# Optimization experiments

Hardware: AMD Instinct MI355X
Metric: run time of the kernel (lower is better)

Reference implementation:

```python
import jax, jax.numpy as jnp
import numpy as np

B, S, DIM = 2, 2048, 2048
H, DH = 16, 128
FF = 4 * DIM
EPS = 1e-5


def layer_norm(x, w, b, eps=EPS):
    m = jnp.mean(x, axis=-1, keepdims=True)
    v = jnp.mean(jnp.square(x - m), axis=-1, keepdims=True)
    return (x - m) * jax.lax.rsqrt(v + eps) * w + b


def apply_rotary(x, cos, sin):
    # x: [B, H, S, DH]; cos/sin: [S, DH//2]; complex multiply on (even, odd) pairs
    x2 = x.reshape(*x.shape[:-1], DH // 2, 2)
    x0, x1 = x2[..., 0], x2[..., 1]
    c = cos[None, None, :, :]
    s = sin[None, None, :, :]
    r0 = x0 * c - x1 * s
    r1 = x0 * s + x1 * c
    return jnp.stack([r0, r1], axis=-1).reshape(x.shape)


def setup_inputs() -> dict:
    key = jax.random.key(0)
    ks = jax.random.split(key, 16)
    sc = 0.02
    pos = jnp.arange(S, dtype=jnp.float32)[:, None]
    inv_freq = 1.0 / (10000.0 ** (jnp.arange(0, DH // 2, dtype=jnp.float32) / (DH // 2)))
    ang = pos * inv_freq[None, :]
    return {
        "hidden_states": jax.random.normal(ks[0], (B, S, DIM), jnp.float32),
        "freqs_cos": jnp.cos(ang),
        "freqs_sin": jnp.sin(ang),
        "wq": jax.random.normal(ks[1], (DIM, H * DH), jnp.float32) * sc,
        "wk": jax.random.normal(ks[2], (DIM, H * DH), jnp.float32) * sc,
        "wv": jax.random.normal(ks[3], (DIM, H * DH), jnp.float32) * sc,
        "nq_w": jnp.ones((DH,), jnp.float32),
        "nq_b": jnp.zeros((DH,), jnp.float32),
        "nk_w": jnp.ones((DH,), jnp.float32),
        "nk_b": jnp.zeros((DH,), jnp.float32),
        "wo": jax.random.normal(ks[4], (H * DH, DIM), jnp.float32) * sc,
        "bo": jnp.zeros((DIM,), jnp.float32),
        "ln1_w": jnp.ones((DIM,), jnp.float32),
        "ln1_b": jnp.zeros((DIM,), jnp.float32),
        "ln3_w": jnp.ones((DIM,), jnp.float32),
        "ln3_b": jnp.zeros((DIM,), jnp.float32),
        "w1": jax.random.normal(ks[5], (DIM, FF), jnp.float32) * sc,
        "b1": jnp.zeros((FF,), jnp.float32),
        "w2": jax.random.normal(ks[6], (FF, DIM), jnp.float32) * sc,
        "b2": jnp.zeros((DIM,), jnp.float32),
    }


def reference(hidden_states, freqs_cos, freqs_sin, wq, wk, wv, nq_w, nq_b, nk_w, nk_b,
              wo, bo, ln1_w, ln1_b, ln3_w, ln3_b, w1, b1, w2, b2):
    x = hidden_states
    # --- self-attention branch ---
    n = layer_norm(x, ln1_w, ln1_b)                       # [B,S,DIM]
    q = (n @ wq).reshape(B, S, H, DH)
    k = (n @ wk).reshape(B, S, H, DH)
    v = (n @ wv).reshape(B, S, H, DH)
    # per-head QK LayerNorm (norm over dim_head)
    q = layer_norm(q, nq_w, nq_b)
    k = layer_norm(k, nk_w, nk_b)
    q = q.transpose(0, 2, 1, 3)                            # [B,H,S,DH]
    k = k.transpose(0, 2, 1, 3)
    v = v.transpose(0, 2, 1, 3)
    q = apply_rotary(q, freqs_cos, freqs_sin)
    k = apply_rotary(k, freqs_cos, freqs_sin)
    scale = DH ** -0.5
    scores = jnp.einsum("bhqd,bhkd->bhqk", q, k) * scale   # [B,H,S,S]
    probs = jax.nn.softmax(scores, axis=-1)
    attn = jnp.einsum("bhqk,bhkd->bhqd", probs, v)         # [B,H,S,DH]
    attn = attn.transpose(0, 2, 1, 3).reshape(B, S, H * DH)
    x = x + (attn @ wo + bo)
    # --- feed-forward branch ---
    n = layer_norm(x, ln3_w, ln3_b)
    h = jax.nn.gelu(n @ w1 + b1, approximate=False)
    x = x + (h @ w2 + b2)
    return x
```

## Files before the change

### kernel.cpp

```cpp
#include <hip/hip_runtime.h>
#include <hip/hip_bf16.h>
#include <stdint.h>

typedef __hip_bfloat16 bf16;
typedef float v4f __attribute__((ext_vector_type(4)));
typedef short v8s __attribute__((ext_vector_type(8)));

#define DEV __device__ __forceinline__

DEV float b2f(bf16 x) { return __bfloat162float(x); }
DEV bf16 f2b(float x) { return __float2bfloat16(x); }

DEV void load4(const float* p, float* f) {
  float4 t = *(const float4*)p;
  f[0] = t.x; f[1] = t.y; f[2] = t.z; f[3] = t.w;
}
DEV void load4(const bf16* p, float* f) {
  union { uint2 u; bf16 h[4]; } t;
  t.u = *(const uint2*)p;
#pragma unroll
  for (int i = 0; i < 4; i++) f[i] = b2f(t.h[i]);
}
DEV void load8(const float* p, float* f) {
  float4 a = ((const float4*)p)[0], b = ((const float4*)p)[1];
  f[0] = a.x; f[1] = a.y; f[2] = a.z; f[3] = a.w;
  f[4] = b.x; f[5] = b.y; f[6] = b.z; f[7] = b.w;
}
DEV void load8(const bf16* p, float* f) {
  union { uint4 u; bf16 h[8]; } t;
  t.u = *(const uint4*)p;
#pragma unroll
  for (int i = 0; i < 8; i++) f[i] = b2f(t.h[i]);
}
DEV void store4(bf16* p, const float* f) {
  union { uint2 u; bf16 h[4]; } t;
#pragma unroll
  for (int i = 0; i < 4; i++) t.h[i] = f2b(f[i]);
  *(uint2*)p = t.u;
}
DEV void store4(float* p, const float* f) {
  *(float4*)p = make_float4(f[0], f[1], f[2], f[3]);
}

DEV void gld_lds16(const bf16* g, bf16* l) {
  auto gp = reinterpret_cast<const __attribute__((address_space(1))) uint32_t*>(
      reinterpret_cast<uintptr_t>(g));
  auto lp = reinterpret_cast<__attribute__((address_space(3))) uint32_t*>(
      reinterpret_cast<uintptr_t>(l));
  __builtin_amdgcn_global_load_lds(gp, lp, 16, 0, 0);
}

template <typename XT>
__global__ __launch_bounds__(256)
void ln2048_kernel(const XT* __restrict__ x, const float* __restrict__ w,
                   const float* __restrict__ b, bf16* __restrict__ y) {
  const int N = 2048;
  int row = blockIdx.x, tid = threadIdx.x;
  const XT* xr = x + (size_t)row * N;
  bf16* yr = y + (size_t)row * N;
  float f[8], s = 0.f, ss = 0.f;
  load8(xr + tid * 8, f);
#pragma unroll
  for (int i = 0; i < 8; i++) { s += f[i]; ss += f[i] * f[i]; }
#pragma unroll
  for (int off = 32; off >= 1; off >>= 1) {
    s  += __shfl_xor(s, off, 64);
    ss += __shfl_xor(ss, off, 64);
  }
  __shared__ float red0[4], red1[4];
  int wv = tid >> 6;
  if ((tid & 63) == 0) { red0[wv] = s; red1[wv] = ss; }
  __syncthreads();
  s  = red0[0] + red0[1] + red0[2] + red0[3];
  ss = red1[0] + red1[1] + red1[2] + red1[3];
  float mean = s * (1.f / N);
  float var  = ss * (1.f / N) - mean * mean;
  float inv  = rsqrtf(var + 1e-5f);
  float wf[8], bf_[8];
  load8(w + tid * 8, wf);
  load8(b + tid * 8, bf_);
  union { uint4 u; bf16 h[8]; } vo;
#pragma unroll
  for (int i = 0; i < 8; i++)
    vo.h[i] = f2b((f[i] - mean) * inv * wf[i] + bf_[i]);
  ((uint4*)yr)[tid] = vo.u;
}

__global__ __launch_bounds__(256)
void headln_rope_kernel(bf16* __restrict__ qb, bf16* __restrict__ kb,
                        const float* __restrict__ nqw, const float* __restrict__ nqb,
                        const float* __restrict__ nkw, const float* __restrict__ nkb,
                        const float* __restrict__ fcos, const float* __restrict__ fsin) {
  int bid = blockIdx.x;
  bf16* qk; const float* w; const float* b;
  if (bid < 16384) { qk = qb; w = nqw; b = nqb; }
  else             { qk = kb; w = nkw; b = nkb; bid -= 16384; }
  int tid = threadIdx.x;
  int wv = tid >> 6, ln = tid & 63;
  int idx = bid * 4 + wv;
  int row = idx >> 4, h = idx & 15;
  int srow = row & 2047;
  bf16* p = qk + (size_t)row * 2048 + h * 128 + ln * 2;
  union { unsigned int u; bf16 h2[2]; } v;
  v.u = *(const unsigned int*)p;
  float x0 = b2f(v.h2[0]), x1 = b2f(v.h2[1]);
  float s = x0 + x1, ss = x0 * x0 + x1 * x1;
#pragma unroll
  for (int off = 32; off >= 1; off >>= 1) {
    s  += __shfl_xor(s, off, 64);
    ss += __shfl_xor(ss, off, 64);
  }
  float mean = s * (1.f / 128.f);
  float var  = ss * (1.f / 128.f) - mean * mean;
  float inv  = rsqrtf(var + 1e-5f);
  float w0 = w[ln * 2], w1 = w[ln * 2 + 1];
  float b0 = b[ln * 2], b1 = b[ln * 2 + 1];
  x0 = (x0 - mean) * inv * w0 + b0;
  x1 = (x1 - mean) * inv * w1 + b1;
  float c  = fcos[srow * 64 + ln];
  float sn = fsin[srow * 64 + ln];
  v.h2[0] = f2b(x0 * c - x1 * sn);
  v.h2[1] = f2b(x0 * sn + x1 * c);
  *(unsigned int*)p = v.u;
}

__global__ __launch_bounds__(256)
void convT_kernel(const float* __restrict__ src, bf16* __restrict__ dst,
                  int K, int N) {
  __shared__ float T[64][65];
  int n0 = blockIdx.x * 64, k0 = blockIdx.y * 64;
  int t = threadIdx.x;
  int tr = t >> 4, tc4 = (t & 15) * 4;
#pragma unroll
  for (int it = 0; it < 4; it++) {
    float4 v = *(const float4*)&src[(size_t)(k0 + tr + 16 * it) * N + n0 + tc4];
    T[tr + 16 * it][tc4 + 0] = v.x;
    T[tr + 16 * it][tc4 + 1] = v.y;
    T[tr + 16 * it][tc4 + 2] = v.z;
    T[tr + 16 * it][tc4 + 3] = v.w;
  }
  __syncthreads();
#pragma unroll
  for (int it = 0; it < 4; it++) {
    int n = tr + 16 * it;
    union { uint2 u; bf16 h[4]; } o;
#pragma unroll
    for (int c = 0; c < 4; c++) o.h[c] = f2b(T[tc4 + c][n]);
    *(uint2*)&dst[(size_t)(n0 + n) * K + k0 + tc4] = o.u;
  }
}

template <int EPI, typename RT, typename OT>
__global__ __launch_bounds__(256, 2)
void mfma_gemm_kernel(const bf16* __restrict__ A, const bf16* __restrict__ BT,
                      OT* __restrict__ C, const float* __restrict__ bias,
                      const RT* __restrict__ res, int M, int N, int K,
                      int ldc_log2, size_t seg_stride) {
  __shared__ __align__(16) bf16 As[128 * 32];
  __shared__ __align__(16) bf16 Bs[128 * 32];
  int tid = threadIdx.x;
  int lane = tid & 63, wave = tid >> 6;
  int wr = wave >> 1, wc = wave & 1;

  int nbx = gridDim.x;
  int bid = blockIdx.y * nbx + blockIdx.x;
  int nwg = nbx * gridDim.y;
  int cpx = nwg >> 3;
  int swz = (bid & 7) * cpx + (bid >> 3);
  int m0 = (swz / nbx) * 128, n0 = (swz % nbx) * 128;

  int ls_row = lane >> 2;
  int ls_k   = (lane & 3) * 8;
  int t0 = 2 * wave, t1 = 2 * wave + 1;
  const bf16* gA0 = A  + (size_t)(m0 + 16 * t0 + ls_row) * K + ls_k;
  const bf16* gA1 = A  + (size_t)(m0 + 16 * t1 + ls_row) * K + ls_k;
  const bf16* gB0 = BT + (size_t)(n0 + 16 * t0 + ls_row) * K + ls_k;
  const bf16* gB1 = BT + (size_t)(n0 + 16 * t1 + ls_row) * K + ls_k;
  bf16* lA0 = As + t0 * 512;
  bf16* lA1 = As + t1 * 512;
  bf16* lB0 = Bs + t0 * 512;
  bf16* lB1 = Bs + t1 * 512;

  int fr = lane & 15, fk = (lane >> 4) * 8;
  const bf16* pA = As + (wr * 64 + fr) * 32 + fk;
  const bf16* pB = Bs + (wc * 64 + fr) * 32 + fk;

  v4f acc[4][4];
#pragma unroll
  for (int i = 0; i < 4; i++)
#pragma unroll
    for (int j = 0; j < 4; j++) acc[i][j] = (v4f){0.f, 0.f, 0.f, 0.f};

  for (int k0 = 0; k0 < K; k0 += 32) {
    __syncthreads();
    gld_lds16(gA0, lA0); gld_lds16(gA1, lA1);
    gld_lds16(gB0, lB0); gld_lds16(gB1, lB1);
    gA0 += 32; gA1 += 32; gB0 += 32; gB1 += 32;
    __syncthreads();
    v8s af[4], bfr[4];
#pragma unroll
    for (int i = 0; i < 4; i++) af[i]  = *(const v8s*)(pA + i * 16 * 32);
#pragma unroll
    for (int j = 0; j < 4; j++) bfr[j] = *(const v8s*)(pB + j * 16 * 32);
#pragma unroll
    for (int i = 0; i < 4; i++)
#pragma unroll
      for (int j = 0; j < 4; j++)
        acc[i][j] = __builtin_amdgcn_mfma_f32_16x16x32_bf16(af[i], bfr[j],
                                                            acc[i][j], 0, 0, 0);
  }

  int rq = (lane >> 4) * 4;
  int ldm = 1 << ldc_log2;
#pragma unroll
  for (int j = 0; j < 4; j++) {
    int n = n0 + wc * 64 + j * 16 + (lane & 15);
    float bb = (EPI >= 1) ? bias[n] : 0.f;
    size_t cseg = (size_t)(n >> ldc_log2) * seg_stride + (n & (ldm - 1));
#pragma unroll
    for (int i = 0; i < 4; i++) {
#pragma unroll
      for (int r = 0; r < 4; r++) {
        int m = m0 + wr * 64 + i * 16 + rq + r;
        float val = acc[i][j][r] + bb;
        if (EPI == 2)
          val = 0.5f * val * (1.f + erff(val * 0.70710678118654752f));
        if (EPI == 1) {
          if constexpr (__is_same(RT, float)) val += res[(size_t)m * N + n];
          else                                val += b2f(res[(size_t)m * N + n]);
        }
        size_t cix = cseg + ((size_t)m << ldc_log2);
        if constexpr (__is_same(OT, float)) C[cix] = val;
        else                                C[cix] = f2b(val);
      }
    }
  }
}

template <int EPI, typename RT, typename OT>
__global__ __launch_bounds__(256)
void gemm_kernel(const bf16* __restrict__ A, const float* __restrict__ Bm,
                 OT* __restrict__ C, const float* __restrict__ bias,
                 const RT* __restrict__ res, int M, int N, int K) {
  const int BK = 32;
  __shared__ __align__(16) float As[BK][68];
  __shared__ __align__(16) float Bs[BK][68];
  int tid = threadIdx.x;
  int bm = blockIdx.y, bn = blockIdx.x;
  int tx = tid & 15, ty = tid >> 4;
  int am = tid >> 2, ak8 = (tid & 3) * 8;
  int bkr = tid >> 3, bn8 = (tid & 7) * 8;
  const bf16* Aptr = A + (size_t)(bm * 64 + am) * K + ak8;
  const float* Bptr = Bm + (size_t)bkr * N + bn * 64 + bn8;
  float acc[4][4] = {};
  for (int k0 = 0; k0 < K; k0 += BK) {
    float av[8], bv[8];
    load8(Aptr, av);
    load8(Bptr, bv);
    __syncthreads();
#pragma unroll
    for (int j = 0; j < 8; j++) As[ak8 + j][am] = av[j];
#pragma unroll
    for (int j = 0; j < 8; j++) Bs[bkr][bn8 + j] = bv[j];
    __syncthreads();
    Aptr += BK;
    Bptr += (size_t)BK * N;
#pragma unroll 8
    for (int kk = 0; kk < BK; kk++) {
      float a0[4], b0[4];
      *(float4*)a0 = *(const float4*)&As[kk][ty * 4];
      *(float4*)b0 = *(const float4*)&Bs[kk][tx * 4];
#pragma unroll
      for (int i = 0; i < 4; i++)
#pragma unroll
        for (int j = 0; j < 4; j++)
          acc[i][j] += a0[i] * b0[j];
    }
  }
  int m0 = bm * 64 + ty * 4, n0 = bn * 64 + tx * 4;
#pragma unroll
  for (int i = 0; i < 4; i++) {
    float r4[4];
#pragma unroll
    for (int j = 0; j < 4; j++) r4[j] = acc[i][j];
    if (EPI >= 1) {
      float bb[4];
      load4(bias + n0, bb);
#pragma unroll
      for (int j = 0; j < 4; j++) r4[j] += bb[j];
    }
    if (EPI == 2) {
#pragma unroll
      for (int j = 0; j < 4; j++)
        r4[j] = 0.5f * r4[j] * (1.f + erff(r4[j] * 0.70710678118654752f));
    }
    if (EPI == 1) {
      float rr[4];
      load4(res + (size_t)(m0 + i) * N + n0, rr);
#pragma unroll
      for (int j = 0; j < 4; j++) r4[j] += rr[j];
    }
    store4(&C[(size_t)(m0 + i) * N + n0], r4);
  }
}

#define VSWZ(r) (((((r) >> 3) ^ (r)) & 7) << 4)

__global__ __launch_bounds__(256, 2)
void attn_kernel(const bf16* __restrict__ q, const bf16* __restrict__ k,
                 const bf16* __restrict__ v, bf16* __restrict__ o) {
  const int S = 2048, HD = 2048;
  __shared__ __align__(16) char smem[57856];
  char* Ks0 = smem;
  char* Ks1 = smem + 16384;
  char* VtB = smem + 32768;
  char* PB  = smem + 49152;
  float* Lp = (float*)(smem + 57344);

  int id = blockIdx.x;
  int swzb = (id & 7) * 128 + (id >> 3);
  int bh = swzb >> 5, qb = swzb & 31;
  int q0 = qb * 64;
  size_t base = (size_t)(bh >> 4) * S * HD + (size_t)(bh & 15) * 128;

  int tid = threadIdx.x;
  int lane = tid & 63, wave = tid >> 6;
  int wr = wave >> 1, wc = wave & 1;
  int fr = lane & 15, fg = lane >> 4;

  if (tid < 128) Lp[tid] = 0.f;

  union V4U { uint4 u; bf16 h[8]; };
  int vr0 = (tid & 15) * 4, vd0 = (tid >> 4) * 8;

#pragma unroll
  for (int t = 0; t < 4; t++) {
    int ti = wave * 4 + t;
    int r = ti * 4 + fg;
    int cb = (fr * 16) ^ ((r & 7) << 4);
    gld_lds16(q + base + (size_t)(q0 + r) * HD + (cb >> 1), (bf16*)Ks0 + ti * 512);
    gld_lds16(k + base + (size_t)r * HD + (cb >> 1), (bf16*)Ks1 + ti * 512);
  }
  V4U vA[4], vB[4];
#pragma unroll
  for (int j = 0; j < 4; j++)
    vA[j].u = *(const uint4*)&v[base + (size_t)(vr0 + j) * HD + vd0];
  __syncthreads();

  v8s qfrag[2][4];
#pragma unroll
  for (int i = 0; i < 2; i++)
#pragma unroll
    for (int kk = 0; kk < 4; kk++) {
      int row = wr * 32 + i * 16 + fr;
      int off = row * 256 + ((kk * 64 + fg * 16) ^ ((row & 7) << 4));
      qfrag[i][kk] = *(const v8s*)(Ks0 + off);
    }
  __syncthreads();

  v4f oacc[2][4];
#pragma unroll
  for (int i = 0; i < 2; i++)
#pragma unroll
    for (int j = 0; j < 4; j++) oacc[i][j] = (v4f){0.f, 0.f, 0.f, 0.f};

  const float scale = 0.08838834764831845f;

#define ATTN_TILE(KT, KCUR, KNXT, VCUR, VNXT, STAGE_NEXT)                     \
  {                                                                           \
    _Pragma("unroll")                                                         \
    for (int c = 0; c < 8; c++) {                                             \
      int d = vd0 + c;                                                        \
      union { uint2 u2; bf16 hh[4]; } pk;                                     \
      _Pragma("unroll")                                                       \
      for (int j = 0; j < 4; j++) pk.hh[j] = VCUR[j].h[c];                    \
      *(uint2*)(VtB + d * 128 + ((vr0 * 2) ^ VSWZ(d))) = pk.u2;               \
    }                                                                         \
    if (STAGE_NEXT) {                                                         \
      _Pragma("unroll")                                                       \
      for (int t = 0; t < 4; t++) {                                           \
        int ti = wave * 4 + t;                                                \
        int r = ti * 4 + fg;                                                  \
        int cb = (fr * 16) ^ ((r & 7) << 4);                                  \
        gld_lds16(k + base + (size_t)((KT) + 64 + r) * HD + (cb >> 1),        \
                  (bf16*)(KNXT) + ti * 512);                                  \
      }                                                                       \
      _Pragma("unroll")                                                       \
      for (int j = 0; j < 4; j++)                                             \
        VNXT[j].u =                                                           \
            *(const uint4*)&v[base + (size_t)((KT) + 64 + vr0 + j) * HD + vd0]; \
    }                                                                         \
    v4f sacc[2][2];                                                           \
    _Pragma("unroll")                                                         \
    for (int i = 0; i < 2; i++)                                               \
      _Pragma("unroll")                                                       \
      for (int j = 0; j < 2; j++) sacc[i][j] = (v4f){0.f, 0.f, 0.f, 0.f};     \
    __builtin_amdgcn_s_setprio(1);                                            \
    _Pragma("unroll")                                                         \
    for (int kk = 0; kk < 4; kk++) {                                          \
      v8s kf[2];                                                              \
      _Pragma("unroll")                                                       \
      for (int j = 0; j < 2; j++) {                                           \
        int row = wc * 32 + j * 16 + fr;                                      \
        int off = row * 256 + ((kk * 64 + fg * 16) ^ ((row & 7) << 4));       \
        kf[j] = *(const v8s*)((KCUR) + off);                                  \
      }                                                                       \
      _Pragma("unroll")                                                       \
      for (int i = 0; i < 2; i++)                                             \
        _Pragma("unroll")                                                     \
        for (int j = 0; j < 2; j++)                                           \
          sacc[i][j] = __builtin_amdgcn_mfma_f32_16x16x32_bf16(               \
              qfrag[i][kk], kf[j], sacc[i][j], 0, 0, 0);                      \
    }                                                                         \
    __builtin_amdgcn_s_setprio(0);                                            \
    _Pragma("unroll")                                                         \
    for (int i = 0; i < 2; i++)                                               \
      _Pragma("unroll")                                                       \
      for (int r = 0; r < 4; r++) {                                           \
        int qrow = wr * 32 + i * 16 + fg * 4 + r;                             \
        float e0 = __expf(sacc[i][0][r] * scale);                             \
        float e1 = __expf(sacc[i][1][r] * scale);                             \
        int sw = VSWZ(qrow);                                                  \
        int c0 = wc * 64 + fr * 2;                                            \
        *(bf16*)(PB + qrow * 128 + (c0 ^ sw)) = f2b(e0);                      \
        *(bf16*)(PB + qrow * 128 + ((c0 + 32) ^ sw)) = f2b(e1);               \
        float s_ = e0 + e1;                                                   \
        s_ += __shfl_xor(s_, 1, 64);                                          \
        s_ += __shfl_xor(s_, 2, 64);                                          \
        s_ += __shfl_xor(s_, 4, 64);                                          \
        s_ += __shfl_xor(s_, 8, 64);                                          \
        if (fr == 0) Lp[wc * 64 + qrow] += s_;                                \
      }                                                                       \
    __syncthreads();                                                          \
    __builtin_amdgcn_s_setprio(1);                                            \
    _Pragma("unroll")                                                         \
    for (int kk2 = 0; kk2 < 2; kk2++) {                                       \
      v8s pf[2], vf[4];                                                       \
      _Pragma("unroll")                                                       \
      for (int i = 0; i < 2; i++) {                                           \
        int row = wr * 32 + i * 16 + fr;                                      \
        int off = row * 128 + ((kk2 * 64 + fg * 16) ^ VSWZ(row));             \
        pf[i] = *(const v8s*)(PB + off);                                      \
      }                                                                       \
      _Pragma("unroll")                                                       \
      for (int j = 0; j < 4; j++) {                                           \
        int row = wc * 64 + j * 16 + fr;                                      \
        int off = row * 128 + ((kk2 * 64 + fg * 16) ^ VSWZ(row));             \
        vf[j] = *(const v8s*)(VtB + off);                                     \
      }                                                                       \
      _Pragma("unroll")                                                       \
      for (int i = 0; i < 2; i++)                                             \
        _Pragma("unroll")                                                     \
        for (int j = 0; j < 4; j++)                                           \
          oacc[i][j] = __builtin_amdgcn_mfma_f32_16x16x32_bf16(               \
              pf[i], vf[j], oacc[i][j], 0, 0, 0);                             \
    }                                                                         \
    __builtin_amdgcn_s_setprio(0);                                            \
    __syncthreads();                                                          \
  }

  for (int tp = 0; tp < 16; tp++) {
    int kt = tp * 128;
    ATTN_TILE(kt, Ks1, Ks0, vA, vB, true);
    ATTN_TILE(kt + 64, Ks0, Ks1, vB, vA, (tp < 15));
  }
#undef ATTN_TILE

#pragma unroll
  for (int i = 0; i < 2; i++)
#pragma unroll
    for (int r = 0; r < 4; r++) {
      int qrow = wr * 32 + i * 16 + fg * 4 + r;
      float linv = 1.f / (Lp[qrow] + Lp[64 + qrow]);
#pragma unroll
      for (int j = 0; j < 4; j++) {
        int d = wc * 64 + j * 16 + fr;
        o[base + (size_t)(q0 + qrow) * HD + d] = f2b(oacc[i][j][r] * linv);
      }
    }
}

extern "C" void kernel_launch(void* const* d_in, const int* in_sizes, int n_in,
                              void* d_out, int out_size, void* d_ws, size_t ws_size,
                              hipStream_t stream) {
  (void)in_sizes; (void)n_in; (void)out_size;
  const float* x    = (const float*)d_in[0];
  const float* fcos = (const float*)d_in[1];
  const float* fsin = (const float*)d_in[2];
  const float* wq   = (const float*)d_in[3];
  const float* wk   = (const float*)d_in[4];
  const float* wv   = (const float*)d_in[5];
  const float* nqw  = (const float*)d_in[6];
  const float* nqb  = (const float*)d_in[7];
  const float* nkw  = (const float*)d_in[8];
  const float* nkb  = (const float*)d_in[9];
  const float* wo   = (const float*)d_in[10];
  const float* bo   = (const float*)d_in[11];
  const float* ln1w = (const float*)d_in[12];
  const float* ln1b = (const float*)d_in[13];
  const float* ln3w = (const float*)d_in[14];
  const float* ln3b = (const float*)d_in[15];
  const float* w1   = (const float*)d_in[16];
  const float* b1   = (const float*)d_in[17];
  const float* w2   = (const float*)d_in[18];
  const float* b2   = (const float*)d_in[19];
  float* out = (float*)d_out;

  const size_t SEG = (size_t)4096 * 2048;
  bf16* base = (bf16*)d_ws;
  bf16* q        = base + 0 * SEG;
  bf16* k        = base + 1 * SEG;
  bf16* v        = base + 2 * SEG;
  bf16* n1       = base + 3 * SEG;
  bf16* attn_out = base + 3 * SEG;
  bf16* x2       = base + 4 * SEG;
  bf16* n3       = base + 5 * SEG;
  bf16* h        = base + 0 * SEG;

  dim3 blk(256);
  ln2048_kernel<float><<<4096, blk, 0, stream>>>(x, ln1w, ln1b, n1);

  bool mfma_path = ws_size >= (size_t)128 * 1024 * 1024;
  if (mfma_path) {
    bf16* W = base + 6 * SEG;
    bf16* wqT = W;
    bf16* wkT = W + 4 * 1024 * 1024;
    bf16* wvT = W + 8 * 1024 * 1024;
    bf16* woT = W;
    bf16* w1T = W;
    bf16* w2T = W;

    dim3 cg22(32, 32);
    dim3 g16(16, 32);
    dim3 g48(48, 32);
    dim3 g64(64, 32);

    convT_kernel<<<cg22, blk, 0, stream>>>(wq, wqT, 2048, 2048);
    convT_kernel<<<cg22, blk, 0, stream>>>(wk, wkT, 2048, 2048);
    convT_kernel<<<cg22, blk, 0, stream>>>(wv, wvT, 2048, 2048);
    mfma_gemm_kernel<0, float, bf16><<<g48, blk, 0, stream>>>(n1, wqT, q, nullptr, nullptr, 4096, 6144, 2048, 11, SEG);
    headln_rope_kernel<<<32768, blk, 0, stream>>>(q, k, nqw, nqb, nkw, nkb, fcos, fsin);
    attn_kernel<<<1024, blk, 0, stream>>>(q, k, v, attn_out);
    convT_kernel<<<cg22, blk, 0, stream>>>(wo, woT, 2048, 2048);
    mfma_gemm_kernel<1, float, bf16><<<g16, blk, 0, stream>>>(attn_out, woT, x2, bo, x, 4096, 2048, 2048, 11, 0);
    ln2048_kernel<bf16><<<4096, blk, 0, stream>>>(x2, ln3w, ln3b, n3);
    convT_kernel<<<dim3(128, 32), blk, 0, stream>>>(w1, w1T, 2048, 8192);
    mfma_gemm_kernel<2, float, bf16><<<g64, blk, 0, stream>>>(n3, w1T, h, b1, nullptr, 4096, 8192, 2048, 13, 0);
    convT_kernel<<<dim3(32, 128), blk, 0, stream>>>(w2, w2T, 8192, 2048);
    mfma_gemm_kernel<1, bf16, float><<<g16, blk, 0, stream>>>(h, w2T, out, b2, x2, 4096, 2048, 8192, 11, 0);
  } else {
    dim3 g2048(32, 64), g8192(128, 64);
    gemm_kernel<0, float, bf16><<<g2048, blk, 0, stream>>>(n1, wq, q, nullptr, nullptr, 4096, 2048, 2048);
    gemm_kernel<0, float, bf16><<<g2048, blk, 0, stream>>>(n1, wk, k, nullptr, nullptr, 4096, 2048, 2048);
    gemm_kernel<0, float, bf16><<<g2048, blk, 0, stream>>>(n1, wv, v, nullptr, nullptr, 4096, 2048, 2048);
    headln_rope_kernel<<<32768, blk, 0, stream>>>(q, k, nqw, nqb, nkw, nkb, fcos, fsin);
    attn_kernel<<<1024, blk, 0, stream>>>(q, k, v, attn_out);
    gemm_kernel<1, float, bf16><<<g2048, blk, 0, stream>>>(attn_out, wo, x2, bo, x, 4096, 2048, 2048);
    ln2048_kernel<bf16><<<4096, blk, 0, stream>>>(x2, ln3w, ln3b, n3);
    gemm_kernel<2, float, bf16><<<g8192, blk, 0, stream>>>(n3, w1, h, b1, nullptr, 4096, 8192, 2048);
    gemm_kernel<1, bf16, float><<<g2048, blk, 0, stream>>>(h, w2, out, b2, x2, 4096, 2048, 8192);
  }
}
```

Before: 1.018 ms.

## Double K-step per iteration and stage bf16 epilogue through swizzled LDS

The MFMA GEMM main loop now loads 64 K-elements per barrier pair into two LDS halves, so it runs half as many __syncthreads per K and issues more global loads before each wait. For bf16 outputs, the epilogue writes results into a swizzled LDS tile and then stores 16-byte vectors per row instead of scattered 2-byte stores. This doubles LDS use to 32KB, which may limit occupancy at two workgroups per CU, and the vector-store path assumes 8-column chunks never cross an ldc segment boundary.

```diff
diff --git a/kernel.cpp b/kernel.cpp
--- a/kernel.cpp
+++ b/kernel.cpp
@@ -156,8 +156,11 @@
                       OT* __restrict__ C, const float* __restrict__ bias,
                       const RT* __restrict__ res, int M, int N, int K,
                       int ldc_log2, size_t seg_stride) {
-  __shared__ __align__(16) bf16 As[128 * 32];
-  __shared__ __align__(16) bf16 Bs[128 * 32];
+  __shared__ __align__(16) char smem[32768];
+  bf16* As_lo = (bf16*)smem;
+  bf16* As_hi = As_lo + 4096;
+  bf16* Bs_lo = As_lo + 8192;
+  bf16* Bs_hi = As_lo + 12288;
   int tid = threadIdx.x;
   int lane = tid & 63, wave = tid >> 6;
   int wr = wave >> 1, wc = wave & 1;
@@ -176,14 +179,14 @@
   const bf16* gA1 = A  + (size_t)(m0 + 16 * t1 + ls_row) * K + ls_k;
   const bf16* gB0 = BT + (size_t)(n0 + 16 * t0 + ls_row) * K + ls_k;
   const bf16* gB1 = BT + (size_t)(n0 + 16 * t1 + ls_row) * K + ls_k;
-  bf16* lA0 = As + t0 * 512;
-  bf16* lA1 = As + t1 * 512;
-  bf16* lB0 = Bs + t0 * 512;
-  bf16* lB1 = Bs + t1 * 512;
+  bf16* lA0lo = As_lo + t0 * 512;  bf16* lA1lo = As_lo + t1 * 512;
+  bf16* lA0hi = As_hi + t0 * 512;  bf16* lA1hi = As_hi + t1 * 512;
+  bf16* lB0lo = Bs_lo + t0 * 512;  bf16* lB1lo = Bs_lo + t1 * 512;
+  bf16* lB0hi = Bs_hi + t0 * 512;  bf16* lB1hi = Bs_hi + t1 * 512;
 
   int fr = lane & 15, fk = (lane >> 4) * 8;
-  const bf16* pA = As + (wr * 64 + fr) * 32 + fk;
-  const bf16* pB = Bs + (wc * 64 + fr) * 32 + fk;
+  int fA = (wr * 64 + fr) * 32 + fk;
+  int fB = (wc * 64 + fr) * 32 + fk;
 
   v4f acc[4][4];
 #pragma unroll
@@ -191,48 +194,101 @@
 #pragma unroll
     for (int j = 0; j < 4; j++) acc[i][j] = (v4f){0.f, 0.f, 0.f, 0.f};
 
-  for (int k0 = 0; k0 < K; k0 += 32) {
+  for (int k0 = 0; k0 < K; k0 += 64) {
     __syncthreads();
-    gld_lds16(gA0, lA0); gld_lds16(gA1, lA1);
-    gld_lds16(gB0, lB0); gld_lds16(gB1, lB1);
-    gA0 += 32; gA1 += 32; gB0 += 32; gB1 += 32;
+    gld_lds16(gA0,      lA0lo); gld_lds16(gA1,      lA1lo);
+    gld_lds16(gA0 + 32, lA0hi); gld_lds16(gA1 + 32, lA1hi);
+    gld_lds16(gB0,      lB0lo); gld_lds16(gB1,      lB1lo);
+    gld_lds16(gB0 + 32, lB0hi); gld_lds16(gB1 + 32, lB1hi);
+    gA0 += 64; gA1 += 64; gB0 += 64; gB1 += 64;
     __syncthreads();
-    v8s af[4], bfr[4];
-#pragma unroll
-    for (int i = 0; i < 4; i++) af[i]  = *(const v8s*)(pA + i * 16 * 32);
-#pragma unroll
-    for (int j = 0; j < 4; j++) bfr[j] = *(const v8s*)(pB + j * 16 * 32);
-#pragma unroll
-    for (int i = 0; i < 4; i++)
-#pragma unroll
-      for (int j = 0; j < 4; j++)
-        acc[i][j] = __builtin_amdgcn_mfma_f32_16x16x32_bf16(af[i], bfr[j],
-                                                            acc[i][j], 0, 0, 0);
+    {
+      v8s af[4], bfr[4];
+#pragma unroll
+      for (int i = 0; i < 4; i++) af[i]  = *(const v8s*)(As_lo + fA + i * 512);
+#pragma unroll
+      for (int j = 0; j < 4; j++) bfr[j] = *(const v8s*)(Bs_lo + fB + j * 512);
+#pragma unroll
+      for (int i = 0; i < 4; i++)
+#pragma unroll
+        for (int j = 0; j < 4; j++)
+          acc[i][j] = __builtin_amdgcn_mfma_f32_16x16x32_bf16(af[i], bfr[j],
+                                                              acc[i][j], 0, 0, 0);
+    }
+    {
+      v8s af[4], bfr[4];
+#pragma unroll
+      for (int i = 0; i < 4; i++) af[i]  = *(const v8s*)(As_hi + fA + i * 512);
+#pragma unroll
+      for (int j = 0; j < 4; j++) bfr[j] = *(const v8s*)(Bs_hi + fB + j * 512);
+#pragma unroll
+      for (int i = 0; i < 4; i++)
+#pragma unroll
+        for (int j = 0; j < 4; j++)
+          acc[i][j] = __builtin_amdgcn_mfma_f32_16x16x32_bf16(af[i], bfr[j],
+                                                              acc[i][j], 0, 0, 0);
+    }
   }
 
   int rq = (lane >> 4) * 4;
   int ldm = 1 << ldc_log2;
-#pragma unroll
-  for (int j = 0; j < 4; j++) {
-    int n = n0 + wc * 64 + j * 16 + (lane & 15);
-    float bb = (EPI >= 1) ? bias[n] : 0.f;
-    size_t cseg = (size_t)(n >> ldc_log2) * seg_stride + (n & (ldm - 1));
-#pragma unroll
-    for (int i = 0; i < 4; i++) {
-#pragma unroll
-      for (int r = 0; r < 4; r++) {
-        int m = m0 + wr * 64 + i * 16 + rq + r;
-        float val = acc[i][j][r] + bb;
-        if (EPI == 2)
-          val = 0.5f * val * (1.f + erff(val * 0.70710678118654752f));
-        if (EPI == 1) {
-          if constexpr (__is_same(RT, float)) val += res[(size_t)m * N + n];
-          else                                val += b2f(res[(size_t)m * N + n]);
+  if constexpr (__is_same(OT, float)) {
+#pragma unroll
+    for (int j = 0; j < 4; j++) {
+      int n = n0 + wc * 64 + j * 16 + fr;
+      float bb = (EPI >= 1) ? bias[n] : 0.f;
+      size_t cseg = (size_t)(n >> ldc_log2) * seg_stride + (n & (ldm - 1));
+#pragma unroll
+      for (int i = 0; i < 4; i++) {
+#pragma unroll
+        for (int r = 0; r < 4; r++) {
+          int m = m0 + wr * 64 + i * 16 + rq + r;
+          float val = acc[i][j][r] + bb;
+          if (EPI == 2)
+            val = 0.5f * val * (1.f + erff(val * 0.70710678118654752f));
+          if (EPI == 1) {
+            if constexpr (__is_same(RT, float)) val += res[(size_t)m * N + n];
+            else                                val += b2f(res[(size_t)m * N + n]);
+          }
+          C[cseg + ((size_t)m << ldc_log2)] = val;
         }
-        size_t cix = cseg + ((size_t)m << ldc_log2);
-        if constexpr (__is_same(OT, float)) C[cix] = val;
-        else                                C[cix] = f2b(val);
       }
+    }
+  } else {
+    __syncthreads();
+#pragma unroll
+    for (int j = 0; j < 4; j++) {
+      int col = wc * 64 + j * 16 + fr;
+      int n = n0 + col;
+      float bb = (EPI >= 1) ? bias[n] : 0.f;
+#pragma unroll
+      for (int i = 0; i < 4; i++) {
+#pragma unroll
+        for (int r = 0; r < 4; r++) {
+          int m = m0 + wr * 64 + i * 16 + rq + r;
+          float val = acc[i][j][r] + bb;
+          if (EPI == 2)
+            val = 0.5f * val * (1.f + erff(val * 0.70710678118654752f));
+          if (EPI == 1) {
+            if constexpr (__is_same(RT, float)) val += res[(size_t)m * N + n];
+            else                                val += b2f(res[(size_t)m * N + n]);
+          }
+          int row = wr * 64 + i * 16 + rq + r;
+          int byteoff = row * 256 + ((((col >> 3) ^ (row & 7))) << 4) + ((col & 7) << 1);
+          *(bf16*)(smem + byteoff) = f2b(val);
+        }
+      }
+    }
+    __syncthreads();
+    int row = tid >> 1, half = tid & 1;
+    size_t gm = (size_t)(m0 + row) << ldc_log2;
+#pragma unroll
+    for (int it = 0; it < 8; it++) {
+      int coln = half * 64 + it * 8;
+      int n = n0 + coln;
+      size_t cseg = (size_t)(n >> ldc_log2) * seg_stride + (n & (ldm - 1));
+      uint4 val = *(uint4*)(smem + row * 256 + ((((coln >> 3) ^ (row & 7))) << 4));
+      *(uint4*)&C[cseg + gm] = val;
     }
   }
 }
```

Result: faster. 990.3 us (-2.7%).
